# Performance work log

Measured on AMD Instinct MI355X. Metric: run time of the kernel, lower is better.

Reference implementation:

```python
import jax, jax.numpy as jnp
import numpy as np

SIGMA = 1.0   # noise std (unit-variance synthetic input)
P = 11        # patch size p1
K = 16        # number of similar patches k1
WIN = 65      # search window w (odd)
S = 3         # reference-patch stride
ALPHA = 0.5   # n2n alpha


def _unfold(x, ksize, stride):
    # (N,1,H,W) -> (N, ksize*ksize, Ho, Wo); kernel positions row-major (== torch F.unfold for C=1)
    return jax.lax.conv_general_dilated_patches(
        x, (ksize, ksize), (stride, stride), 'VALID',
        dimension_numbers=('NCHW', 'OIHW', 'NCHW'))


def block_matching(x, k, p, w, s):
    N, _, H, W = x.shape
    v = w // 2
    assert (H - p + 1) % s == 1 and (W - p + 1) % s == 1  # no edge-case branches needed
    Href = (H - p) // s + 1
    Wref = (W - p) // s + 1
    x_pad = jnp.pad(x, ((0, 0), (0, 0), (v, v), (v, v)))  # zero pad; invalid candidates masked below
    # |patch|^2 / p^2 at every position of the padded image (== F.avg_pool2d(x**2, p))
    sq = jax.lax.reduce_window(x_pad * x_pad, 0.0, jax.lax.add,
                               (1, 1, p, p), (1, 1, 1, 1), 'VALID') / (p * p)
    norms = _unfold(sq, 2 * v + 1, s)                                  # (N,(2v+1)^2,Href,Wref)
    norms = norms.reshape(N, 2 * v + 1, 2 * v + 1, Href, Wref).transpose(0, 3, 4, 1, 2)
    lw = _unfold(x_pad, 2 * v + p, s) / p                              # (N,(2v+p)^2,Href,Wref)
    lw = lw.reshape(N, 2 * v + p, 2 * v + p, Href, Wref).transpose(0, 3, 4, 1, 2)
    G = N * Href * Wref
    lw = lw.reshape(1, G, 2 * v + p, 2 * v + p)
    ref = lw[0, :, v:-v, v:-v][:, None]                                # (G,1,p,p) reference patches
    sp = jax.lax.conv_general_dilated(
        lw, ref, (1, 1), 'VALID',
        dimension_numbers=('NCHW', 'OIHW', 'NCHW'),
        feature_group_count=G)                                         # (1,G,2v+1,2v+1)
    dist = norms.reshape(1, G, 2 * v + 1, 2 * v + 1) - 2.0 * sp
    dist = dist.reshape(N, Href, Wref, 2 * v + 1, 2 * v + 1)
    # mask candidate patches that fall outside the original image (torch uses NaN padding + topk)
    offs = jnp.arange(-v, v + 1)
    hr = jnp.arange(Href) * s
    wr = jnp.arange(Wref) * s
    row_ok = (hr[:, None] + offs >= 0) & (hr[:, None] + offs <= H - p)  # (Href, 2v+1)
    col_ok = (wr[:, None] + offs >= 0) & (wr[:, None] + offs <= W - p)  # (Wref, 2v+1)
    valid = row_ok[:, None, :, None] & col_ok[None, :, None, :]
    dist = jnp.where(valid[None], dist, jnp.inf)
    dist = dist.at[..., v, v].set(-jnp.inf)                            # reference patch always kept
    dist = dist.reshape(N, Href, Wref, (2 * v + 1) ** 2)
    _, idx = jax.lax.top_k(-dist, k)                                   # k smallest distances
    ind_row = idx // (2 * v + 1) - v
    ind_col = idx % (2 * v + 1) - v
    ind = (ind_row + hr[None, :, None, None]) * (W - p + 1) + (ind_col + wr[None, None, :, None])
    return ind.reshape(N, -1)                                          # (N, Href*Wref*k)


def gather_groups(y, indices, k, p):
    N = y.shape[0]
    uf = _unfold(y, p, 1).reshape(N, p * p, -1)                        # (N, n, (H-p+1)(W-p+1))
    Yg = jnp.take_along_axis(uf, indices[:, None, :], axis=2)          # (N, n, L*k)
    L = indices.shape[1] // k
    return Yg.reshape(N, p * p, L, k).transpose(0, 2, 3, 1)            # (N, L, k, n)


def denoise1(Y, sigma):
    # method='n2n', constraints='affine'
    N, B, k, n = Y.shape
    D = n * sigma ** 2
    E = n * ALPHA ** 2 * sigma ** 2
    Ik = jnp.eye(k, dtype=Y.dtype)
    Q = Y @ jnp.swapaxes(Y, 2, 3) + E * Ik                             # (N,B,k,k), SPD
    Lc = jnp.linalg.cholesky(Q)
    Ikb = jnp.broadcast_to(Ik, Q.shape)
    Z = jax.scipy.linalg.solve_triangular(Lc, Ikb, lower=True)
    Qinv = jax.scipy.linalg.solve_triangular(jnp.swapaxes(Lc, 2, 3), Z, lower=False)
    Qinv1 = jnp.sum(Qinv, axis=3, keepdims=True)
    Qinv2 = jnp.sum(Qinv1, axis=2, keepdims=True)
    theta = Ik - (Qinv - (Qinv1 @ jnp.swapaxes(Qinv1, 2, 3)) / Qinv2) * (D + E)
    theta = jnp.swapaxes(theta, 2, 3)
    X_hat = theta @ Y
    weights = 1.0 / jnp.clip(jnp.sum(theta * theta, axis=3, keepdims=True), 1.0 / k, 1.0)
    return X_hat, weights


def _fold(x, H, W, p):
    # inverse of unfold: sum overlapping p x p patches back onto the image grid
    N, n, _ = x.shape
    Hp, Wp = H - p + 1, W - p + 1
    x = x.reshape(N, p, p, Hp, Wp)
    out = jnp.zeros((N, 1, H, W), x.dtype)
    for a in range(p):
        for b in range(p):
            out = out.at[:, 0, a:a + Hp, b:b + Wp].add(x[:, a, b])
    return out


def aggregate(X_hat, weights, indices, H, W, p):
    N, L, k, n = X_hat.shape
    X = (X_hat * weights).reshape(N, L * k, n).transpose(0, 2, 1)      # (N, n, L*k)
    Wt = jnp.broadcast_to(weights, (N, L, k, n)).reshape(N, L * k, n).transpose(0, 2, 1)
    Lfull = (H - p + 1) * (W - p + 1)
    def scat(vals, idx):
        return jnp.zeros((n, Lfull), vals.dtype).at[:, idx].add(vals)
    X_sum = jax.vmap(scat)(X, indices)
    W_sum = jax.vmap(scat)(Wt, indices)
    return _fold(X_sum, H, W, p) / _fold(W_sum, H, W, p)


def _forward(y):
    N, C, H, W = y.shape
    indices = block_matching(y, K, P, WIN, S)
    Yg = gather_groups(y, indices, K, P)
    X_hat, weights = denoise1(Yg, SIGMA)
    return aggregate(X_hat, weights, indices, H, W, P)


def setup_inputs():
    key = jax.random.key(0)
    y = jax.random.normal(key, (4, 1, 128, 128), dtype=jnp.float32)
    return {"y": y}


def reference(y):
    return _forward(y)
```

## Files before the change

### kernel.cpp

```cpp
#include <hip/hip_runtime.h>
#include <math.h>

#define HH 128
#define WW 128
#define NIMG 4
#define PP 11
#define KSIM 16
#define STRIDE_S 3
#define VRAD 32
#define WINW 65
#define NTASK (WINW*9)
#define HREF 40
#define WREF 40
#define NPOS 118
#define WROWS 75
#define WPITCH 84
#define NGROUP (NIMG*HREF*WREF)
#define EPS_E 30.25f
#define DE_C 151.25f
#define INFD 3.0e38f
#define RTASK 292
#define THREC 152

__global__ __launch_bounds__(256, 5)
void bm_kernel(const float* __restrict__ y, int* __restrict__ inds)
{
    __shared__ float win[WROWS][WPITCH];
    __shared__ float swv[4];
    __shared__ int   swi[4];

    const int blk = blockIdx.x;
    const int n   = blk / (HREF*WREF);
    const int rem = blk % (HREF*WREF);
    const int hr  = (rem / WREF) * STRIDE_S;
    const int wr  = (rem % WREF) * STRIDE_S;
    const float* img = y + n * HH * WW;
    const int tid = threadIdx.x;

    for (int t = tid; t < WROWS * WPITCH; t += 256) {
        int r = t / WPITCH, c = t % WPITCH;
        int gr = hr - VRAD + r, gc = wr - VRAD + c;
        float v = 0.f;
        if (c < WROWS && gr >= 0 && gr < HH && gc >= 0 && gc < WW)
            v = img[gr * WW + gc];
        win[r][c] = v;
    }
    __syncthreads();

    float d[3][8];
#pragma unroll
    for (int s = 0; s < 3; s++)
#pragma unroll
        for (int c = 0; c < 8; c++) d[s][c] = INFD;

#pragma unroll
    for (int s = 0; s < 3; s++) {
        int task = tid + (s << 8);
        if (task < NTASK) {
            int drx = task % WINW;
            int c0  = (task / WINW) * 8;
            int rr  = hr + drx - VRAD;
            bool rowok = (rr >= 0 && rr <= HH - PP);
            if (rowok) {
                float dot[8];
                float colsq[18];
#pragma unroll
                for (int c = 0; c < 8; c++) dot[c] = 0.f;
#pragma unroll
                for (int j2 = 0; j2 < 18; j2++) colsq[j2] = 0.f;
                for (int a = 0; a < PP; a++) {
                    const float4* w4 = reinterpret_cast<const float4*>(&win[drx + a][c0]);
                    float4 A0 = w4[0], A1 = w4[1], A2 = w4[2], A3 = w4[3];
                    float2 A4 = *reinterpret_cast<const float2*>(&win[drx + a][c0 + 16]);
                    float wv[18] = {A0.x,A0.y,A0.z,A0.w, A1.x,A1.y,A1.z,A1.w,
                                    A2.x,A2.y,A2.z,A2.w, A3.x,A3.y,A3.z,A3.w,
                                    A4.x,A4.y};
                    const float4* r4 = reinterpret_cast<const float4*>(&win[VRAD + a][VRAD]);
                    float4 R0 = r4[0], R1 = r4[1];
                    float2 R2 = *reinterpret_cast<const float2*>(&win[VRAD + a][VRAD + 8]);
                    float  R3 = win[VRAD + a][VRAD + 10];
                    float rv[11] = {R0.x,R0.y,R0.z,R0.w, R1.x,R1.y,R1.z,R1.w,
                                    R2.x,R2.y, R3};
#pragma unroll
                    for (int j2 = 0; j2 < 18; j2++) colsq[j2] += wv[j2] * wv[j2];
#pragma unroll
                    for (int b = 0; b < PP; b++) {
#pragma unroll
                        for (int c = 0; c < 8; c++)
                            dot[c] += wv[b + c] * rv[b];
                    }
                }
#pragma unroll
                for (int j2 = 1; j2 < 18; j2++) colsq[j2] += colsq[j2 - 1];
#pragma unroll
                for (int c = 0; c < 8; c++) {
                    int dcx = c0 + c;
                    int cc  = wr + dcx - VRAD;
                    float norm = colsq[c + 10] - (c ? colsq[c - 1] : 0.f);
                    if (dcx < WINW && cc >= 0 && cc <= WW - PP)
                        d[s][c] = norm - 2.f * dot[c];
                }
            }
            if (task == RTASK) d[s][0] = -INFD;
        }
    }

    float lval = INFD; int lidx = 0;
#pragma unroll
    for (int s = 0; s < 3; s++)
#pragma unroll
        for (int c = 0; c < 8; c++)
            if (d[s][c] < lval) { lval = d[s][c]; lidx = (s << 3) | c; }

    for (int sel = 0; sel < KSIM; sel++) {
        float rv = lval;
        int   ri = ((tid + ((lidx >> 3) << 8)) << 3) | (lidx & 7);
#pragma unroll
        for (int off = 32; off > 0; off >>= 1) {
            float ov = __shfl_down(rv, off);
            int   oi = __shfl_down(ri, off);
            if (ov < rv) { rv = ov; ri = oi; }
        }
        if ((tid & 63) == 0) { swv[tid >> 6] = rv; swi[tid >> 6] = ri; }
        __syncthreads();
        float bval = swv[0]; int bidx = swi[0];
#pragma unroll
        for (int w2 = 1; w2 < 4; w2++)
            if (swv[w2] < bval) { bval = swv[w2]; bidx = swi[w2]; }
        if (tid == 0) {
            int task2 = bidx >> 3;
            int drx = task2 % WINW;
            int dcx = (task2 / WINW) * 8 + (bidx & 7);
            inds[blk * KSIM + sel] =
                (hr + drx - VRAD) * NPOS + (wr + dcx - VRAD);
        }
        __syncthreads();
        int otid = (bidx >> 3) & 255;
        if (tid == otid) {
            int code = (((bidx >> 3) >> 8) << 3) | (bidx & 7);
            lval = INFD; lidx = 0;
#pragma unroll
            for (int s = 0; s < 3; s++)
#pragma unroll
                for (int c = 0; c < 8; c++) {
                    if (((s << 3) | c) == code) d[s][c] = INFD;
                    if (d[s][c] < lval) { lval = d[s][c]; lidx = (s << 3) | c; }
                }
        }
    }
}

__global__ __launch_bounds__(256)
void dn_solve(const float* __restrict__ y, const int* __restrict__ inds,
              float* __restrict__ thW)
{
    __shared__ float Qs[4][16][17];
    __shared__ float s1[4][16];
    __shared__ float s2[4];
    __shared__ float wl[4][16];
    __shared__ short pr_[4][16], pc_[4][16];

    const int blk = blockIdx.x;
    const int tid = threadIdx.x;
    const int g0 = blk * 4;

    if (tid < 64) {
        int gq = tid >> 4, m = tid & 15;
        int idx = inds[(g0 + gq) * KSIM + m];
        pr_[gq][m] = (short)(idx / NPOS);
        pc_[gq][m] = (short)(idx % NPOS);
    }
    __syncthreads();

    for (int t = tid; t < 4 * 136; t += 256) {
        int gq = t / 136, e = t % 136;
        int i = (int)((sqrtf(8.f * (float)e + 1.f) - 1.f) * 0.5f + 1e-4f);
        int j = e - i * (i + 1) / 2;
        const float* img = y + ((g0 + gq) / (HREF * WREF)) * HH * WW;
        const float* Pi = img + (int)pr_[gq][i] * WW + (int)pc_[gq][i];
        const float* Pj = img + (int)pr_[gq][j] * WW + (int)pc_[gq][j];
        float s = (i == j) ? EPS_E : 0.f;
        for (int a = 0; a < PP; a++) {
            const float* Ri = Pi + a * WW;
            const float* Rj = Pj + a * WW;
#pragma unroll
            for (int b = 0; b < PP; b++) s += Ri[b] * Rj[b];
        }
        Qs[gq][i][j] = s;
        Qs[gq][j][i] = s;
    }
    __syncthreads();

    const int gq = tid >> 6, ii = (tid >> 2) & 15, jq = tid & 3;
    for (int ks = 0; ks < 16; ks++) {
        float fA = Qs[gq][ii][ks];
        float pv = Qs[gq][ks][ks];
        float rk[4], aij[4];
#pragma unroll
        for (int q = 0; q < 4; q++) {
            rk[q]  = Qs[gq][ks][jq * 4 + q];
            aij[q] = Qs[gq][ii][jq * 4 + q];
        }
        __syncthreads();
        float inv = 1.f / pv;
#pragma unroll
        for (int q = 0; q < 4; q++) {
            int jj = jq * 4 + q;
            float nv;
            if (ii == ks) nv = (jj == ks) ? inv : rk[q] * inv;
            else          nv = (jj == ks) ? -fA * inv : aij[q] - fA * rk[q] * inv;
            Qs[gq][ii][jj] = nv;
        }
        __syncthreads();
    }

    if (jq == 0) {
        float s = 0.f;
#pragma unroll
        for (int b = 0; b < 16; b++) s += Qs[gq][ii][b];
        s1[gq][ii] = s;
    }
    __syncthreads();
    if (ii == 0 && jq == 0) {
        float s = 0.f;
#pragma unroll
        for (int a = 0; a < 16; a++) s += s1[gq][a];
        s2[gq] = s;
    }
    __syncthreads();
    {
        float s1i = s1[gq][ii];
#pragma unroll
        for (int q = 0; q < 4; q++) {
            int jj = jq * 4 + q;
            float t2 = ((ii == jj) ? 1.f : 0.f)
                     - (Qs[gq][ii][jj] - s1i * s1[gq][jj] / s2[gq]) * DE_C;
            Qs[gq][ii][jj] = t2;
        }
    }
    __syncthreads();
    if (jq == 1) {
        float s = 0.f;
#pragma unroll
        for (int m = 0; m < 16; m++) { float t2 = Qs[gq][m][ii]; s += t2 * t2; }
        s = fminf(fmaxf(s, 1.f / 16.f), 1.f);
        wl[gq][ii] = 1.f / s;
    }
    __syncthreads();

    for (int t = tid; t < 4 * THREC; t += 256) {
        int gg = t / THREC, e = t % THREC;
        float v;
        if (e < 136) {
            int i = (int)((sqrtf(8.f * (float)e + 1.f) - 1.f) * 0.5f + 1e-4f);
            int j = e - i * (i + 1) / 2;
            v = Qs[gg][i][j];
        } else {
            v = wl[gg][e - 136];
        }
        thW[(size_t)(g0 + gg) * THREC + e] = v;
    }
}

__global__ __launch_bounds__(512, 1)
void dn_scatter(const float* __restrict__ y, const int* __restrict__ inds,
                const float* __restrict__ thW, float2* __restrict__ nd, int R)
{
    __shared__ float2 acc[84][85];
    __shared__ float  thS[16][THREC];
    __shared__ short  pr_[16][16], pc_[16][16];

    const int blk = blockIdx.x;
    const int n  = blk / 100;
    const int tr = blk % 100;
    const int ti = tr / 10, tj = tr % 10;
    const int r0 = 12 * ti - VRAD, c0 = 12 * tj - VRAD;
    const int tid = threadIdx.x;
    const float* img = y + n * HH * WW;

    if (tid < 256) {
        int g = tid >> 4, m = tid & 15;
        int gg = n * (HREF * WREF) + (ti * 4 + (g >> 2)) * WREF + (tj * 4 + (g & 3));
        int idx = inds[gg * KSIM + m];
        pr_[g][m] = (short)(idx / NPOS);
        pc_[g][m] = (short)(idx % NPOS);
    }
    for (int t = tid; t < 16 * THREC; t += 512) {
        int g = t / THREC, e = t % THREC;
        int gg = n * (HREF * WREF) + (ti * 4 + (g >> 2)) * WREF + (tj * 4 + (g & 3));
        thS[g][e] = thW[(size_t)gg * THREC + e];
    }
    for (int t = tid; t < 84 * 85; t += 512)
        ((float2*)acc)[t] = make_float2(0.f, 0.f);
    __syncthreads();

    const int g6 = tid >> 5, sub = tid & 31, rq = sub >> 2, pq = sub & 3;
    int bs[16];
#pragma unroll
    for (int m = 0; m < 16; m++)
        bs[m] = (int)pr_[g6][m] * WW + (int)pc_[g6][m];
    float Ar[2][16]; float wr2[2]; int ar2[2], ac2[2];
#pragma unroll
    for (int k = 0; k < 2; k++) {
        int r = rq * 2 + k;
        float w = thS[g6][136 + r];
#pragma unroll
        for (int m = 0; m < 16; m++) {
            int hi = (m > r) ? m : r, lo = (m > r) ? r : m;
            Ar[k][m] = thS[g6][hi * (hi + 1) / 2 + lo] * w;
        }
        wr2[k] = w;
        ar2[k] = (int)pr_[g6][r] - r0;
        ac2[k] = (int)pc_[g6][r] - c0;
    }

#pragma unroll 1
    for (int t = 0; t < 31; t++) {
        int px = pq * 31 + t;
        if (px < 121) {
            int dra = px / 11, dca = px % 11;
            const int off = dra * WW + dca;
            float yv[16];
#pragma unroll
            for (int m = 0; m < 16; m++) yv[m] = img[bs[m] + off];
#pragma unroll
            for (int k = 0; k < 2; k++) {
                float xw = 0.f;
#pragma unroll
                for (int m = 0; m < 16; m++) xw += Ar[k][m] * yv[m];
                float* cell = (float*)&acc[ar2[k] + dra][ac2[k] + dca];
                __hip_atomic_fetch_add(cell,     xw,
                    __ATOMIC_RELAXED, __HIP_MEMORY_SCOPE_WORKGROUP);
                __hip_atomic_fetch_add(cell + 1, wr2[k],
                    __ATOMIC_RELAXED, __HIP_MEMORY_SCOPE_WORKGROUP);
            }
        }
    }
    __syncthreads();

    float2* ndI = nd + ((size_t)(blk & (R - 1)) * NIMG + n) * HH * WW;
    for (int t = tid; t < 84 * 84; t += 512) {
        int rr = t / 84, cc = t % 84;
        float2 vv = acc[rr][cc];
        if (vv.y != 0.f) {
            int px = (r0 + rr) * WW + (c0 + cc);
#if defined(__has_builtin) && __has_builtin(__builtin_amdgcn_global_atomic_fadd_v2f32)
            typedef float v2f __attribute__((ext_vector_type(2)));
            __builtin_amdgcn_global_atomic_fadd_v2f32((v2f*)&ndI[px], (v2f){vv.x, vv.y});
#else
            atomicAdd(&ndI[px].x, vv.x);
            atomicAdd(&ndI[px].y, vv.y);
#endif
        }
    }
}

__global__ __launch_bounds__(256)
void fin_kernel(const float2* __restrict__ nd, float* __restrict__ out, int R)
{
    int t = blockIdx.x * 256 + threadIdx.x;
    if (t < NIMG * HH * WW) {
        float sn = 0.f, sd = 0.f;
        for (int r = 0; r < R; r++) {
            float2 vv = nd[(size_t)r * NIMG * HH * WW + t];
            sn += vv.x; sd += vv.y;
        }
        out[t] = sn / sd;
    }
}

extern "C" void kernel_launch(void* const* d_in, const int* in_sizes, int n_in,
                              void* d_out, int out_size, void* d_ws, size_t ws_size,
                              hipStream_t stream)
{
    const float* y = (const float*)d_in[0];
    float* out = (float*)d_out;

    size_t perRep = (size_t)NIMG * HH * WW * sizeof(float2);
    size_t indsB  = (size_t)NGROUP * KSIM * sizeof(int);
    size_t thWB   = (size_t)NGROUP * THREC * sizeof(float);
    int R = 1;
    while (R < 4 && perRep * (size_t)(R * 2) + indsB + thWB <= ws_size) R <<= 1;

    float2* nd   = (float2*)d_ws;
    int*    inds = (int*)((char*)d_ws + perRep * (size_t)R);
    float*  thW  = (float*)((char*)inds + indsB);

    hipMemsetAsync(nd, 0, perRep * (size_t)R, stream);
    bm_kernel<<<NGROUP, 256, 0, stream>>>(y, inds);
    dn_solve<<<NGROUP / 4, 256, 0, stream>>>(y, inds, thW);
    dn_scatter<<<NIMG * 100, 512, 0, stream>>>(y, inds, thW, nd, R);
    fin_kernel<<<(NIMG * HH * WW + 255) / 256, 256, 0, stream>>>(nd, out, R);
}
```

Baseline: 445.3 us.

## Stage patches in LDS for Gram matrix and restructure scatter per pixel

In dn_solve, the 16 similar patches per group are first copied into shared memory as padded rows, and the Gram matrix is then computed with float4 LDS reads instead of strided global loads. In dn_scatter, each group's weighted A matrix is prebuilt in shared memory. Each thread now handles one (group, pixel) pair: it reads each patch value once and accumulates all 16 outputs, rather than each thread recomputing per-row products over 31 pixels. This cuts redundant global image reads but uses more LDS and registers (xw[16]), and the launch-bounds minimum-blocks hint is dropped.

```diff
diff --git a/kernel.cpp b/kernel.cpp
--- a/kernel.cpp
+++ b/kernel.cpp
@@ -154,6 +154,7 @@
 void dn_solve(const float* __restrict__ y, const int* __restrict__ inds,
               float* __restrict__ thW)
 {
+    __shared__ float Yp[4][16][124];
     __shared__ float Qs[4][16][17];
     __shared__ float s1[4][16];
     __shared__ float s2[4];
@@ -170,21 +171,32 @@
         pr_[gq][m] = (short)(idx / NPOS);
         pc_[gq][m] = (short)(idx % NPOS);
     }
+    if (tid < 192) {
+        int gq = tid / 48, m = (tid / 3) % 16, e = tid % 3;
+        Yp[gq][m][121 + e] = 0.f;
+    }
+    __syncthreads();
+
+    for (int t = tid; t < 4 * 16 * 121; t += 256) {
+        int gq = t / 1936, m = (t / 121) % 16, j = t % 121;
+        int a = j / PP, b = j % PP;
+        const float* img = y + ((g0 + gq) / (HREF * WREF)) * HH * WW;
+        Yp[gq][m][j] = img[((int)pr_[gq][m] + a) * WW + (int)pc_[gq][m] + b];
+    }
     __syncthreads();
 
     for (int t = tid; t < 4 * 136; t += 256) {
         int gq = t / 136, e = t % 136;
         int i = (int)((sqrtf(8.f * (float)e + 1.f) - 1.f) * 0.5f + 1e-4f);
         int j = e - i * (i + 1) / 2;
-        const float* img = y + ((g0 + gq) / (HREF * WREF)) * HH * WW;
-        const float* Pi = img + (int)pr_[gq][i] * WW + (int)pc_[gq][i];
-        const float* Pj = img + (int)pr_[gq][j] * WW + (int)pc_[gq][j];
+        const float4* Yi = reinterpret_cast<const float4*>(&Yp[gq][i][0]);
+        const float4* Yj = reinterpret_cast<const float4*>(&Yp[gq][j][0]);
         float s = (i == j) ? EPS_E : 0.f;
-        for (int a = 0; a < PP; a++) {
-            const float* Ri = Pi + a * WW;
-            const float* Rj = Pj + a * WW;
-#pragma unroll
-            for (int b = 0; b < PP; b++) s += Ri[b] * Rj[b];
+#pragma unroll
+        for (int q = 0; q < 31; q++) {
+            float4 xi = Yi[q], xj = Yj[q];
+            s += xi.x * xj.x; s += xi.y * xj.y;
+            s += xi.z * xj.z; s += xi.w * xj.w;
         }
         Qs[gq][i][j] = s;
         Qs[gq][j][i] = s;
@@ -262,13 +274,15 @@
     }
 }
 
-__global__ __launch_bounds__(512, 1)
+__global__ __launch_bounds__(512)
 void dn_scatter(const float* __restrict__ y, const int* __restrict__ inds,
                 const float* __restrict__ thW, float2* __restrict__ nd, int R)
 {
     __shared__ float2 acc[84][85];
-    __shared__ float  thS[16][THREC];
-    __shared__ short  pr_[16][16], pc_[16][16];
+    __shared__ float  Athw[16][16][16];
+    __shared__ float  wlS[16][16];
+    __shared__ int    pOff[16][16];
+    __shared__ int    pBase[16][16];
 
     const int blk = blockIdx.x;
     const int n  = blk / 100;
@@ -282,56 +296,52 @@
         int g = tid >> 4, m = tid & 15;
         int gg = n * (HREF * WREF) + (ti * 4 + (g >> 2)) * WREF + (tj * 4 + (g & 3));
         int idx = inds[gg * KSIM + m];
-        pr_[g][m] = (short)(idx / NPOS);
-        pc_[g][m] = (short)(idx % NPOS);
-    }
-    for (int t = tid; t < 16 * THREC; t += 512) {
-        int g = t / THREC, e = t % THREC;
+        int pr = idx / NPOS, pc = idx % NPOS;
+        pOff[g][m]  = (pr - r0) * 85 + (pc - c0);
+        pBase[g][m] = pr * WW + pc;
+        wlS[g][m]   = thW[(size_t)gg * THREC + 136 + m];
+    }
+    __syncthreads();
+    for (int t = tid; t < 16 * 256; t += 512) {
+        int g = t >> 8, m = (t >> 4) & 15, r = t & 15;
         int gg = n * (HREF * WREF) + (ti * 4 + (g >> 2)) * WREF + (tj * 4 + (g & 3));
-        thS[g][e] = thW[(size_t)gg * THREC + e];
+        int hi = (m > r) ? m : r, lo = (m > r) ? r : m;
+        Athw[g][m][r] = thW[(size_t)gg * THREC + hi * (hi + 1) / 2 + lo] * wlS[g][r];
     }
     for (int t = tid; t < 84 * 85; t += 512)
         ((float2*)acc)[t] = make_float2(0.f, 0.f);
     __syncthreads();
 
-    const int g6 = tid >> 5, sub = tid & 31, rq = sub >> 2, pq = sub & 3;
-    int bs[16];
-#pragma unroll
-    for (int m = 0; m < 16; m++)
-        bs[m] = (int)pr_[g6][m] * WW + (int)pc_[g6][m];
-    float Ar[2][16]; float wr2[2]; int ar2[2], ac2[2];
-#pragma unroll
-    for (int k = 0; k < 2; k++) {
-        int r = rq * 2 + k;
-        float w = thS[g6][136 + r];
-#pragma unroll
-        for (int m = 0; m < 16; m++) {
-            int hi = (m > r) ? m : r, lo = (m > r) ? r : m;
-            Ar[k][m] = thS[g6][hi * (hi + 1) / 2 + lo] * w;
-        }
-        wr2[k] = w;
-        ar2[k] = (int)pr_[g6][r] - r0;
-        ac2[k] = (int)pc_[g6][r] - c0;
-    }
-
-#pragma unroll 1
-    for (int t = 0; t < 31; t++) {
-        int px = pq * 31 + t;
-        if (px < 121) {
-            int dra = px / 11, dca = px % 11;
-            const int off = dra * WW + dca;
-            float yv[16];
-#pragma unroll
-            for (int m = 0; m < 16; m++) yv[m] = img[bs[m] + off];
-#pragma unroll
-            for (int k = 0; k < 2; k++) {
-                float xw = 0.f;
-#pragma unroll
-                for (int m = 0; m < 16; m++) xw += Ar[k][m] * yv[m];
-                float* cell = (float*)&acc[ar2[k] + dra][ac2[k] + dca];
-                __hip_atomic_fetch_add(cell,     xw,
+    for (int it = 0; it < 4; it++) {
+        int task = tid + it * 512;
+        if (task < 16 * 121) {
+            int g = task / 121, px = task % 121;
+            int dra = px / PP, dca = px % PP;
+            const int off  = dra * WW + dca;
+            const int offA = dra * 85 + dca;
+            float xw[16];
+#pragma unroll
+            for (int r = 0; r < 16; r++) xw[r] = 0.f;
+#pragma unroll
+            for (int m = 0; m < 16; m++) {
+                float yv = img[pBase[g][m] + off];
+                const float4* Arow = reinterpret_cast<const float4*>(&Athw[g][m][0]);
+                float4 A0 = Arow[0], A1 = Arow[1], A2 = Arow[2], A3 = Arow[3];
+                xw[0]  += A0.x * yv; xw[1]  += A0.y * yv;
+                xw[2]  += A0.z * yv; xw[3]  += A0.w * yv;
+                xw[4]  += A1.x * yv; xw[5]  += A1.y * yv;
+                xw[6]  += A1.z * yv; xw[7]  += A1.w * yv;
+                xw[8]  += A2.x * yv; xw[9]  += A2.y * yv;
+                xw[10] += A2.z * yv; xw[11] += A2.w * yv;
+                xw[12] += A3.x * yv; xw[13] += A3.y * yv;
+                xw[14] += A3.z * yv; xw[15] += A3.w * yv;
+            }
+#pragma unroll
+            for (int r = 0; r < 16; r++) {
+                float* cell = (float*)acc + 2 * (pOff[g][r] + offA);
+                __hip_atomic_fetch_add(cell,     xw[r],
                     __ATOMIC_RELAXED, __HIP_MEMORY_SCOPE_WORKGROUP);
-                __hip_atomic_fetch_add(cell + 1, wr2[k],
+                __hip_atomic_fetch_add(cell + 1, wlS[g][r],
                     __ATOMIC_RELAXED, __HIP_MEMORY_SCOPE_WORKGROUP);
             }
         }
```

New measurement: 427.8 us (median of 2 runs). 3.9% less time.
